# Kernel tuning notes

Hardware: AMD Instinct MI355X
Metric: run time of the kernel (lower is better)

## Reference

```python
import jax, jax.numpy as jnp
import numpy as np

N = 20000          # nodes
E_RAND = 320000    # random edges (avg degree 16)
E = E_RAND + N     # + self loops (no 0-in-degree nodes)
F_IN = 128
H1, D1 = 8, 32     # layer-1 heads / per-head dim
N_CLS = 40
NEG_SLOPE = 0.2


def setup_inputs() -> dict:
    key = jax.random.key(0)
    ks = jax.random.split(key, 9)
    x = jax.random.normal(ks[0], (N, F_IN), jnp.float32)
    src = jnp.concatenate([jax.random.randint(ks[1], (E_RAND,), 0, N),
                           jnp.arange(N)]).astype(jnp.int32)
    dst = jnp.concatenate([jax.random.randint(ks[2], (E_RAND,), 0, N),
                           jnp.arange(N)]).astype(jnp.int32)
    W1 = jax.random.normal(ks[3], (F_IN, H1 * D1), jnp.float32) / np.sqrt(F_IN)
    attn_l1 = jax.random.normal(ks[4], (H1, D1), jnp.float32) * 0.1
    attn_r1 = jax.random.normal(ks[5], (H1, D1), jnp.float32) * 0.1
    W2 = jax.random.normal(ks[6], (H1 * D1, N_CLS), jnp.float32) / np.sqrt(H1 * D1)
    attn_l2 = jax.random.normal(ks[7], (1, N_CLS), jnp.float32) * 0.1
    attn_r2 = jax.random.normal(ks[8], (1, N_CLS), jnp.float32) * 0.1
    return {"x": x, "W1": W1, "attn_l1": attn_l1, "attn_r1": attn_r1,
            "W2": W2, "attn_l2": attn_l2, "attn_r2": attn_r2,
            "src": src, "dst": dst}


def gat_layer(h, W, attn_l, attn_r, src, dst, n_nodes):
    """DGL GATConv (aggr='mean' path), eval mode (dropout = identity)."""
    H, D = attn_l.shape
    ft = (h @ W).reshape(-1, H, D)                 # [N, H, D]
    el = jnp.sum(ft * attn_l, axis=-1)             # [N, H]
    er = jnp.sum(ft * attn_r, axis=-1)             # [N, H]
    e = jax.nn.leaky_relu(el[src] + er[dst], NEG_SLOPE)   # [E, H]
    # ragged softmax over incoming edges of each dst node
    m = jax.ops.segment_max(e, dst, num_segments=n_nodes)
    m = jnp.where(jnp.isfinite(m), m, 0.0)         # guard empty segments
    ex = jnp.exp(e - m[dst])                       # [E, H]
    s = jax.ops.segment_sum(ex, dst, num_segments=n_nodes)
    alpha = ex / jnp.maximum(s[dst], 1e-16)        # [E, H]
    # weighted sum of src features
    out = jax.ops.segment_sum(ft[src] * alpha[:, :, None], dst,
                              num_segments=n_nodes)  # [N, H, D]
    return out


def reference(x, W1, attn_l1, attn_r1, W2, attn_l2, attn_r2, src, dst):
    h = gat_layer(x, W1, attn_l1, attn_r1, src, dst, N)   # [N, 8, 32]
    h = jax.nn.relu(h).reshape(N, H1 * D1)                # flatten(1)
    out = gat_layer(h, W2, attn_l2, attn_r2, src, dst, N) # [N, 1, 40]
    return out.mean(axis=1)                               # [N, 40]
```

## Files before the change

kernel.cpp:

```cpp
#include <hip/hip_runtime.h>
#include <hip/hip_fp16.h>

#define FIN 128
#define F1 256
#define H1N 8
#define D1N 32
#define NCLS 40
#define FT2P 64
#define NEG 0.2f

static __device__ __forceinline__ float leaky(float x){ return x >= 0.f ? x : NEG*x; }

__global__ void k_hist(const int* __restrict__ dst, int* __restrict__ deg, int E){
    int e = blockIdx.x*256 + threadIdx.x;
    if (e < E) atomicAdd(&deg[dst[e]], 1);
}

__global__ __launch_bounds__(1024) void k_scan(const int* __restrict__ deg,
                                               int* __restrict__ rowptr,
                                               int n, int E){
    __shared__ int s[1024];
    int t = threadIdx.x;
    int per = (n + 1023) / 1024;
    int base = t * per;
    int sum = 0;
    for (int i = 0; i < per; i++){
        int idx = base + i;
        if (idx < n) sum += deg[idx];
    }
    s[t] = sum;
    __syncthreads();
    for (int off = 1; off < 1024; off <<= 1){
        int v = (t >= off) ? s[t-off] : 0;
        __syncthreads();
        s[t] += v;
        __syncthreads();
    }
    int run = s[t] - sum;
    for (int i = 0; i < per; i++){
        int idx = base + i;
        if (idx < n){ rowptr[idx] = run; run += deg[idx]; }
    }
    if (t == 1023) rowptr[n] = E;
}

__global__ void k_scatter(const int* __restrict__ src, const int* __restrict__ dst,
                          const int* __restrict__ rowptr, int* __restrict__ deg,
                          int* __restrict__ adj, int E){
    int e = blockIdx.x*256 + threadIdx.x;
    if (e < E){
        int d = dst[e];
        int pos = atomicSub(&deg[d], 1) - 1;
        adj[rowptr[d] + pos] = src[e];
    }
}

__global__ __launch_bounds__(256) void k_gemm1(const float* __restrict__ X,
                                               const float* __restrict__ W,
                                               const float* __restrict__ al,
                                               const float* __restrict__ ar,
                                               __half* __restrict__ FT,
                                               float* __restrict__ el,
                                               float* __restrict__ er, int M){
    __shared__ float As[32][68];
    __shared__ float Bs[32][68];
    int t = threadIdx.x;
    int bx = blockIdx.x & 3;
    int by = blockIdx.x >> 2;
    int m0 = by*64, n0 = bx*64;
    int ty = t >> 4, tx = t & 15;
    float acc[4][4] = {};
    for (int k0 = 0; k0 < FIN; k0 += 32){
        #pragma unroll
        for (int p=0;p<2;p++){
            int f = t + p*256;
            int m = f >> 3;
            int kq = f & 7;
            int row = m0 + m;
            float4 v = make_float4(0.f,0.f,0.f,0.f);
            if (row < M) v = *(const float4*)&X[row*FIN + k0 + kq*4];
            As[kq*4+0][m] = v.x; As[kq*4+1][m] = v.y;
            As[kq*4+2][m] = v.z; As[kq*4+3][m] = v.w;
        }
        #pragma unroll
        for (int p=0;p<2;p++){
            int f = t + p*256;
            int kk = f >> 4;
            int nq = f & 15;
            float4 v = *(const float4*)&W[(size_t)(k0+kk)*F1 + n0 + nq*4];
            *(float4*)&Bs[kk][nq*4] = v;
        }
        __syncthreads();
        #pragma unroll
        for (int kk=0; kk<32; kk++){
            float4 a4 = *(const float4*)&As[kk][ty*4];
            float4 b4 = *(const float4*)&Bs[kk][tx*4];
            float av[4] = {a4.x,a4.y,a4.z,a4.w};
            float bv[4] = {b4.x,b4.y,b4.z,b4.w};
            #pragma unroll
            for (int r=0;r<4;r++)
                #pragma unroll
                for (int c=0;c<4;c++)
                    acc[r][c] = fmaf(av[r], bv[c], acc[r][c]);
        }
        __syncthreads();
    }
    int h = (bx<<1) + (tx>>3);
    int basew = h*D1N + (tx&7)*4;
    float4 wl = *(const float4*)&al[basew];
    float4 wr = *(const float4*)&ar[basew];
    float pl[4], pr[4];
    #pragma unroll
    for (int r=0;r<4;r++){
        pl[r] = acc[r][0]*wl.x + acc[r][1]*wl.y + acc[r][2]*wl.z + acc[r][3]*wl.w;
        pr[r] = acc[r][0]*wr.x + acc[r][1]*wr.y + acc[r][2]*wr.z + acc[r][3]*wr.w;
    }
    #pragma unroll
    for (int msk=1; msk<8; msk<<=1){
        #pragma unroll
        for (int r=0;r<4;r++){
            pl[r] += __shfl_xor(pl[r], msk);
            pr[r] += __shfl_xor(pr[r], msk);
        }
    }
    #pragma unroll
    for (int r=0;r<4;r++){
        int row = m0 + ty*4 + r;
        if (row < M){
            union { uint2 u; __half2 h2[2]; } P;
            P.h2[0] = __floats2half2_rn(acc[r][0], acc[r][1]);
            P.h2[1] = __floats2half2_rn(acc[r][2], acc[r][3]);
            *(uint2*)&FT[(size_t)row*F1 + n0 + tx*4] = P.u;
            if ((tx & 7) == 0){
                el[row*H1N + h] = pl[r];
                er[row*H1N + h] = pr[r];
            }
        }
    }
}

__global__ __launch_bounds__(256) void k_agg1(const __half* __restrict__ FT,
                      const float* __restrict__ el, const float* __restrict__ er,
                      const int* __restrict__ rowptr, const int* __restrict__ adj,
                      float* __restrict__ hout, int n){
    int node = (blockIdx.x*256 + threadIdx.x) >> 6;
    int l = threadIdx.x & 63;
    if (node >= n) return;
    int rs = rowptr[node];
    int deg = rowptr[node+1] - rs;

    int h = l & 7, je = l >> 3;
    float erh = er[node*H1N + h];
    float m = -1e30f, ssum = 0.f;
    for (int j0 = 0; j0 < deg; j0 += 8){
        int j = j0 + je;
        if (j < deg){
            int s = adj[rs + j];
            float e = leaky(el[s*H1N + h] + erh);
            if (e > m){ ssum = ssum*__expf(m - e) + 1.f; m = e; }
            else ssum += __expf(e - m);
        }
    }
    #pragma unroll
    for (int msk=8; msk<64; msk<<=1){
        float m2 = __shfl_xor(m, msk);
        float s2 = __shfl_xor(ssum, msk);
        float nm = fmaxf(m, m2);
        ssum = ssum*__expf(m - nm) + s2*__expf(m2 - nm);
        m = nm;
    }

    int h2 = l >> 3;
    float m2 = __shfl(m, h2);
    float s2 = __shfl(ssum, h2);
    float inv = 1.f / fmaxf(s2, 1e-16f);
    float erh2 = er[node*H1N + h2];
    float ax=0.f, ay=0.f, az=0.f, aw=0.f;
    int j = 0;
    for (; j + 8 <= deg; j += 8){
        int sv[8];
        #pragma unroll
        for (int i=0;i<8;i++) sv[i] = adj[rs+j+i];
        float av[8];
        #pragma unroll
        for (int i=0;i<8;i++)
            av[i] = __expf(leaky(el[sv[i]*H1N + h2] + erh2) - m2);
        #pragma unroll
        for (int i=0;i<8;i++){
            union { uint2 u; __half2 h2v[2]; } U;
            U.u = *(const uint2*)&FT[(size_t)sv[i]*F1 + l*4];
            float2 f01 = __half22float2(U.h2v[0]);
            float2 f23 = __half22float2(U.h2v[1]);
            ax = fmaf(av[i], f01.x, ax); ay = fmaf(av[i], f01.y, ay);
            az = fmaf(av[i], f23.x, az); aw = fmaf(av[i], f23.y, aw);
        }
    }
    for (; j < deg; j++){
        int s = adj[rs + j];
        float a = __expf(leaky(el[s*H1N + h2] + erh2) - m2);
        union { uint2 u; __half2 h2v[2]; } U;
        U.u = *(const uint2*)&FT[(size_t)s*F1 + l*4];
        float2 f01 = __half22float2(U.h2v[0]);
        float2 f23 = __half22float2(U.h2v[1]);
        ax = fmaf(a, f01.x, ax); ay = fmaf(a, f01.y, ay);
        az = fmaf(a, f23.x, az); aw = fmaf(a, f23.y, aw);
    }
    ax *= inv; ay *= inv; az *= inv; aw *= inv;
    *(float4*)&hout[(size_t)node*F1 + l*4] =
        make_float4(fmaxf(ax,0.f), fmaxf(ay,0.f), fmaxf(az,0.f), fmaxf(aw,0.f));
}

__global__ __launch_bounds__(256) void k_gemm2(const float* __restrict__ Hm,
                                               const float* __restrict__ W,
                                               const float* __restrict__ al2,
                                               const float* __restrict__ ar2,
                                               __half* __restrict__ FT2,
                                               float* __restrict__ el2,
                                               float* __restrict__ er2, int M){
    __shared__ float W2s[F1*NCLS];
    __shared__ float hs[128][33];
    int t = threadIdx.x;
    for (int i = t; i < F1*NCLS; i += 256) W2s[i] = W[i];
    int r0 = blockIdx.x*128;
    int rr = t & 63;
    int cg = t >> 6;
    int c0 = cg*10;
    float acc[2][10] = {};
    for (int k0 = 0; k0 < F1; k0 += 32){
        __syncthreads();
        #pragma unroll
        for (int p=0;p<4;p++){
            int f = t + p*256;
            int row = f >> 3;
            int kq = f & 7;
            int gr = r0 + row;
            float4 v = make_float4(0.f,0.f,0.f,0.f);
            if (gr < M) v = *(const float4*)&Hm[(size_t)gr*F1 + k0 + kq*4];
            hs[row][kq*4+0] = v.x; hs[row][kq*4+1] = v.y;
            hs[row][kq*4+2] = v.z; hs[row][kq*4+3] = v.w;
        }
        __syncthreads();
        #pragma unroll
        for (int k=0;k<32;k++){
            float a0 = hs[rr][k], a1 = hs[rr+64][k];
            const float* wp = &W2s[(k0+k)*NCLS + c0];
            #pragma unroll
            for (int c=0;c<10;c+=2){
                float2 w = *(const float2*)&wp[c];
                acc[0][c]   = fmaf(a0, w.x, acc[0][c]);
                acc[0][c+1] = fmaf(a0, w.y, acc[0][c+1]);
                acc[1][c]   = fmaf(a1, w.x, acc[1][c]);
                acc[1][c+1] = fmaf(a1, w.y, acc[1][c+1]);
            }
        }
    }
    float pl[2] = {0.f,0.f}, pr[2] = {0.f,0.f};
    #pragma unroll
    for (int c=0;c<10;c++){
        float a2l = al2[c0+c], a2r = ar2[c0+c];
        pl[0] = fmaf(acc[0][c], a2l, pl[0]); pr[0] = fmaf(acc[0][c], a2r, pr[0]);
        pl[1] = fmaf(acc[1][c], a2l, pl[1]); pr[1] = fmaf(acc[1][c], a2r, pr[1]);
    }
    #pragma unroll
    for (int i=0;i<2;i++){
        int gr = r0 + rr + i*64;
        if (gr < M){
            #pragma unroll
            for (int c=0;c<10;c+=2){
                __half2 hp = __floats2half2_rn(acc[i][c], acc[i][c+1]);
                *(__half2*)&FT2[(size_t)gr*FT2P + c0 + c] = hp;
            }
            atomicAdd(&el2[gr], pl[i]);
            atomicAdd(&er2[gr], pr[i]);
        }
    }
}

__global__ __launch_bounds__(256) void k_agg2(const __half* __restrict__ FT2,
                      const float* __restrict__ el, const float* __restrict__ er,
                      const int* __restrict__ rowptr, const int* __restrict__ adj,
                      float* __restrict__ out, int n){
    int node = (blockIdx.x*256 + threadIdx.x) >> 6;
    int l = threadIdx.x & 63;
    if (node >= n) return;
    int rs = rowptr[node];
    int deg = rowptr[node+1] - rs;
    float ern = er[node];
    float m = -1e30f, ssum = 0.f;
    for (int j = l; j < deg; j += 64){
        int s = adj[rs + j];
        float e = leaky(el[s] + ern);
        if (e > m){ ssum = ssum*__expf(m - e) + 1.f; m = e; }
        else ssum += __expf(e - m);
    }
    #pragma unroll
    for (int msk=1; msk<64; msk<<=1){
        float mm = __shfl_xor(m, msk);
        float s2 = __shfl_xor(ssum, msk);
        float nm = fmaxf(m, mm);
        ssum = ssum*__expf(m - nm) + s2*__expf(mm - nm);
        m = nm;
    }
    float inv = 1.f / fmaxf(ssum, 1e-16f);
    float acc = 0.f;
    int j = 0;
    for (; j + 8 <= deg; j += 8){
        int sv[8];
        #pragma unroll
        for (int i=0;i<8;i++) sv[i] = adj[rs+j+i];
        float av[8];
        #pragma unroll
        for (int i=0;i<8;i++)
            av[i] = __expf(leaky(el[sv[i]] + ern) - m);
        if (l < NCLS){
            #pragma unroll
            for (int i=0;i<8;i++){
                float f = __half2float(FT2[(size_t)sv[i]*FT2P + l]);
                acc = fmaf(av[i], f, acc);
            }
        }
    }
    for (; j < deg; j++){
        int s = adj[rs + j];
        float a = __expf(leaky(el[s] + ern) - m);
        if (l < NCLS) acc = fmaf(a, __half2float(FT2[(size_t)s*FT2P + l]), acc);
    }
    if (l < NCLS) out[(size_t)node*NCLS + l] = acc * inv;
}

extern "C" void kernel_launch(void* const* d_in, const int* in_sizes, int n_in,
                              void* d_out, int out_size, void* d_ws, size_t ws_size,
                              hipStream_t stream){
    const float* x   = (const float*)d_in[0];
    const float* W1  = (const float*)d_in[1];
    const float* al1 = (const float*)d_in[2];
    const float* ar1 = (const float*)d_in[3];
    const float* W2  = (const float*)d_in[4];
    const float* al2 = (const float*)d_in[5];
    const float* ar2 = (const float*)d_in[6];
    const int*   src = (const int*)d_in[7];
    const int*   dst = (const int*)d_in[8];
    int E = in_sizes[7];
    int n = in_sizes[0] / FIN;

    char* ws = (char*)d_ws;
    size_t off = 0;
    auto alloc = [&](size_t bytes)->void*{
        void* p = ws + off; off += (bytes + 255) & ~(size_t)255; return p;
    };
    __half* ft1h  = (__half*)alloc((size_t)n*F1*2);
    float*  hbuf  = (float*)alloc((size_t)n*F1*4);
    __half* ft2h  = (__half*)alloc((size_t)n*FT2P*2);
    float*  el1   = (float*)alloc((size_t)n*H1N*4);
    float*  er1   = (float*)alloc((size_t)n*H1N*4);
    int*    rowptr= (int*)alloc((size_t)(n+1)*4);
    int*    adj   = (int*)alloc((size_t)E*4);
    size_t  z0    = off;
    int*    deg   = (int*)alloc((size_t)n*4);
    float*  el2   = (float*)alloc((size_t)n*4);
    float*  er2   = (float*)alloc((size_t)n*4);
    size_t  z1    = off;

    int nb_e = (E + 255)/256;

    hipMemsetAsync(ws + z0, 0, z1 - z0, stream);
    k_hist   <<<nb_e, 256, 0, stream>>>(dst, deg, E);
    k_scan   <<<1, 1024, 0, stream>>>(deg, rowptr, n, E);
    k_scatter<<<nb_e, 256, 0, stream>>>(src, dst, rowptr, deg, adj, E);

    k_gemm1  <<<((n+63)/64)*4, 256, 0, stream>>>(x, W1, al1, ar1, ft1h, el1, er1, n);
    k_agg1   <<<(n+3)/4, 256, 0, stream>>>(ft1h, el1, er1, rowptr, adj, hbuf, n);

    k_gemm2  <<<(n+127)/128, 256, 0, stream>>>(hbuf, W2, al2, ar2, ft2h, el2, er2, n);
    k_agg2   <<<(n+3)/4, 256, 0, stream>>>(ft2h, el2, er2, rowptr, adj, (float*)d_out, n);
}
```

Before: 245.8 us.

## Fuse layer-2 GEMM into layer-1 aggregation and parallelize the degree scan

The layer-1 aggregation kernel now also multiplies each node's 256-wide ReLU output by W2, held in shared memory as fp16. It writes FT2 and el2/er2 directly, so the fp32 hidden buffer no longer round-trips through global memory and the separate GEMM2 kernel and its atomics are gone. The single-block 1024-thread scan is replaced with a two-kernel multi-block scan. The aggregation kernel now uses a persistent grid-stride loop over 2500 blocks. In exchange, each wave does a serial 256-long dot product per node, W2 is staged per block, and fp16 W2 adds some precision loss.

Result: faster. 212.1 us (-13.7%).

```diff
diff --git a/kernel.cpp b/kernel.cpp
--- a/kernel.cpp
+++ b/kernel.cpp
@@ -7,6 +7,7 @@
 #define D1N 32
 #define NCLS 40
 #define FT2P 64
+#define W2PITCH 260
 #define NEG 0.2f
 
 static __device__ __forceinline__ float leaky(float x){ return x >= 0.f ? x : NEG*x; }
@@ -16,32 +17,34 @@
     if (e < E) atomicAdd(&deg[dst[e]], 1);
 }
 
-__global__ __launch_bounds__(1024) void k_scan(const int* __restrict__ deg,
-                                               int* __restrict__ rowptr,
-                                               int n, int E){
-    __shared__ int s[1024];
+__global__ void k_scan1(const int* __restrict__ deg, int* __restrict__ rowptr,
+                        int* __restrict__ bsum, int n){
+    __shared__ int s[256];
     int t = threadIdx.x;
-    int per = (n + 1023) / 1024;
-    int base = t * per;
-    int sum = 0;
-    for (int i = 0; i < per; i++){
-        int idx = base + i;
-        if (idx < n) sum += deg[idx];
-    }
-    s[t] = sum;
+    int i = blockIdx.x*256 + t;
+    int v = (i < n) ? deg[i] : 0;
+    s[t] = v;
     __syncthreads();
-    for (int off = 1; off < 1024; off <<= 1){
-        int v = (t >= off) ? s[t-off] : 0;
+    for (int off=1; off<256; off<<=1){
+        int y = (t >= off) ? s[t-off] : 0;
         __syncthreads();
-        s[t] += v;
+        if (t >= off) s[t] += y;
         __syncthreads();
     }
-    int run = s[t] - sum;
-    for (int i = 0; i < per; i++){
-        int idx = base + i;
-        if (idx < n){ rowptr[idx] = run; run += deg[idx]; }
-    }
-    if (t == 1023) rowptr[n] = E;
+    if (i < n) rowptr[i] = s[t] - v;
+    if (t == 255) bsum[blockIdx.x] = s[255];
+}
+
+__global__ void k_scan2(int* __restrict__ rowptr, const int* __restrict__ bsum,
+                        int n, int E){
+    int b = blockIdx.x;
+    int l = threadIdx.x & 63;
+    int v = 0;
+    for (int j = l; j < b; j += 64) v += bsum[j];
+    for (int msk=1; msk<64; msk<<=1) v += __shfl_xor(v, msk);
+    int i = b*256 + threadIdx.x;
+    if (i < n) rowptr[i] += v;
+    else if (i == n) rowptr[n] = E;
 }
 
 __global__ void k_scatter(const int* __restrict__ src, const int* __restrict__ dst,
@@ -141,138 +144,113 @@
 
 __global__ __launch_bounds__(256) void k_agg1(const __half* __restrict__ FT,
                       const float* __restrict__ el, const float* __restrict__ er,
+                      const float* __restrict__ W2,
+                      const float* __restrict__ al2, const float* __restrict__ ar2,
                       const int* __restrict__ rowptr, const int* __restrict__ adj,
-                      float* __restrict__ hout, int n){
-    int node = (blockIdx.x*256 + threadIdx.x) >> 6;
-    int l = threadIdx.x & 63;
-    if (node >= n) return;
-    int rs = rowptr[node];
-    int deg = rowptr[node+1] - rs;
-
+                      __half* __restrict__ FT2, float* __restrict__ el2,
+                      float* __restrict__ er2, int n, int nwTot){
+    __shared__ __half W2h[40*W2PITCH];
+    __shared__ float  hst[4][260];
+    int t = threadIdx.x;
+    for (int e = t; e < 256*40; e += 256){
+        int k = e / 40, c = e - k*40;
+        W2h[c*W2PITCH + k] = __float2half_rn(W2[e]);
+    }
+    __syncthreads();
+
+    int w = t >> 6, l = t & 63;
     int h = l & 7, je = l >> 3;
-    float erh = er[node*H1N + h];
-    float m = -1e30f, ssum = 0.f;
-    for (int j0 = 0; j0 < deg; j0 += 8){
-        int j = j0 + je;
-        if (j < deg){
+    int h2 = l >> 3;
+    int c = (l < 40) ? l : (l - 40);
+    float keep = (l < NCLS) ? 1.f : 0.f;
+    float a2l = al2[c], a2r = ar2[c];
+    const __half* wrow = &W2h[c*W2PITCH];
+    float* hp = &hst[w][0];
+
+    for (int node = blockIdx.x*4 + w; node < n; node += nwTot){
+        int rs = rowptr[node];
+        int deg = rowptr[node+1] - rs;
+
+        float erh = er[node*H1N + h];
+        float m = -1e30f, ssum = 0.f;
+        for (int j0 = 0; j0 < deg; j0 += 8){
+            int j = j0 + je;
+            if (j < deg){
+                int s = adj[rs + j];
+                float e = leaky(el[s*H1N + h] + erh);
+                if (e > m){ ssum = ssum*__expf(m - e) + 1.f; m = e; }
+                else ssum += __expf(e - m);
+            }
+        }
+        #pragma unroll
+        for (int msk=8; msk<64; msk<<=1){
+            float m2 = __shfl_xor(m, msk);
+            float s2 = __shfl_xor(ssum, msk);
+            float nm = fmaxf(m, m2);
+            ssum = ssum*__expf(m - nm) + s2*__expf(m2 - nm);
+            m = nm;
+        }
+
+        float m2 = __shfl(m, h2);
+        float s2 = __shfl(ssum, h2);
+        float inv = 1.f / fmaxf(s2, 1e-16f);
+        float erh2 = er[node*H1N + h2];
+        float ax=0.f, ay=0.f, az=0.f, aw=0.f;
+        int j = 0;
+        for (; j + 8 <= deg; j += 8){
+            int sv[8];
+            #pragma unroll
+            for (int i=0;i<8;i++) sv[i] = adj[rs+j+i];
+            float av[8];
+            #pragma unroll
+            for (int i=0;i<8;i++)
+                av[i] = __expf(leaky(el[sv[i]*H1N + h2] + erh2) - m2);
+            #pragma unroll
+            for (int i=0;i<8;i++){
+                union { uint2 u; __half2 h2v[2]; } U;
+                U.u = *(const uint2*)&FT[(size_t)sv[i]*F1 + l*4];
+                float2 f01 = __half22float2(U.h2v[0]);
+                float2 f23 = __half22float2(U.h2v[1]);
+                ax = fmaf(av[i], f01.x, ax); ay = fmaf(av[i], f01.y, ay);
+                az = fmaf(av[i], f23.x, az); aw = fmaf(av[i], f23.y, aw);
+            }
+        }
+        for (; j < deg; j++){
             int s = adj[rs + j];
-            float e = leaky(el[s*H1N + h] + erh);
-            if (e > m){ ssum = ssum*__expf(m - e) + 1.f; m = e; }
-            else ssum += __expf(e - m);
-        }
-    }
-    #pragma unroll
-    for (int msk=8; msk<64; msk<<=1){
-        float m2 = __shfl_xor(m, msk);
-        float s2 = __shfl_xor(ssum, msk);
-        float nm = fmaxf(m, m2);
-        ssum = ssum*__expf(m - nm) + s2*__expf(m2 - nm);
-        m = nm;
-    }
-
-    int h2 = l >> 3;
-    float m2 = __shfl(m, h2);
-    float s2 = __shfl(ssum, h2);
-    float inv = 1.f / fmaxf(s2, 1e-16f);
-    float erh2 = er[node*H1N + h2];
-    float ax=0.f, ay=0.f, az=0.f, aw=0.f;
-    int j = 0;
-    for (; j + 8 <= deg; j += 8){
-        int sv[8];
-        #pragma unroll
-        for (int i=0;i<8;i++) sv[i] = adj[rs+j+i];
-        float av[8];
-        #pragma unroll
-        for (int i=0;i<8;i++)
-            av[i] = __expf(leaky(el[sv[i]*H1N + h2] + erh2) - m2);
-        #pragma unroll
-        for (int i=0;i<8;i++){
+            float a = __expf(leaky(el[s*H1N + h2] + erh2) - m2);
             union { uint2 u; __half2 h2v[2]; } U;
-            U.u = *(const uint2*)&FT[(size_t)sv[i]*F1 + l*4];
+            U.u = *(const uint2*)&FT[(size_t)s*F1 + l*4];
             float2 f01 = __half22float2(U.h2v[0]);
             float2 f23 = __half22float2(U.h2v[1]);
-            ax = fmaf(av[i], f01.x, ax); ay = fmaf(av[i], f01.y, ay);
-            az = fmaf(av[i], f23.x, az); aw = fmaf(av[i], f23.y, aw);
-        }
-    }
-    for (; j < deg; j++){
-        int s = adj[rs + j];
-        float a = __expf(leaky(el[s*H1N + h2] + erh2) - m2);
-        union { uint2 u; __half2 h2v[2]; } U;
-        U.u = *(const uint2*)&FT[(size_t)s*F1 + l*4];
-        float2 f01 = __half22float2(U.h2v[0]);
-        float2 f23 = __half22float2(U.h2v[1]);
-        ax = fmaf(a, f01.x, ax); ay = fmaf(a, f01.y, ay);
-        az = fmaf(a, f23.x, az); aw = fmaf(a, f23.y, aw);
-    }
-    ax *= inv; ay *= inv; az *= inv; aw *= inv;
-    *(float4*)&hout[(size_t)node*F1 + l*4] =
-        make_float4(fmaxf(ax,0.f), fmaxf(ay,0.f), fmaxf(az,0.f), fmaxf(aw,0.f));
-}
-
-__global__ __launch_bounds__(256) void k_gemm2(const float* __restrict__ Hm,
-                                               const float* __restrict__ W,
-                                               const float* __restrict__ al2,
-                                               const float* __restrict__ ar2,
-                                               __half* __restrict__ FT2,
-                                               float* __restrict__ el2,
-                                               float* __restrict__ er2, int M){
-    __shared__ float W2s[F1*NCLS];
-    __shared__ float hs[128][33];
-    int t = threadIdx.x;
-    for (int i = t; i < F1*NCLS; i += 256) W2s[i] = W[i];
-    int r0 = blockIdx.x*128;
-    int rr = t & 63;
-    int cg = t >> 6;
-    int c0 = cg*10;
-    float acc[2][10] = {};
-    for (int k0 = 0; k0 < F1; k0 += 32){
-        __syncthreads();
-        #pragma unroll
-        for (int p=0;p<4;p++){
-            int f = t + p*256;
-            int row = f >> 3;
-            int kq = f & 7;
-            int gr = r0 + row;
-            float4 v = make_float4(0.f,0.f,0.f,0.f);
-            if (gr < M) v = *(const float4*)&Hm[(size_t)gr*F1 + k0 + kq*4];
-            hs[row][kq*4+0] = v.x; hs[row][kq*4+1] = v.y;
-            hs[row][kq*4+2] = v.z; hs[row][kq*4+3] = v.w;
-        }
-        __syncthreads();
-        #pragma unroll
-        for (int k=0;k<32;k++){
-            float a0 = hs[rr][k], a1 = hs[rr+64][k];
-            const float* wp = &W2s[(k0+k)*NCLS + c0];
-            #pragma unroll
-            for (int c=0;c<10;c+=2){
-                float2 w = *(const float2*)&wp[c];
-                acc[0][c]   = fmaf(a0, w.x, acc[0][c]);
-                acc[0][c+1] = fmaf(a0, w.y, acc[0][c+1]);
-                acc[1][c]   = fmaf(a1, w.x, acc[1][c]);
-                acc[1][c+1] = fmaf(a1, w.y, acc[1][c+1]);
-            }
-        }
-    }
-    float pl[2] = {0.f,0.f}, pr[2] = {0.f,0.f};
-    #pragma unroll
-    for (int c=0;c<10;c++){
-        float a2l = al2[c0+c], a2r = ar2[c0+c];
-        pl[0] = fmaf(acc[0][c], a2l, pl[0]); pr[0] = fmaf(acc[0][c], a2r, pr[0]);
-        pl[1] = fmaf(acc[1][c], a2l, pl[1]); pr[1] = fmaf(acc[1][c], a2r, pr[1]);
-    }
-    #pragma unroll
-    for (int i=0;i<2;i++){
-        int gr = r0 + rr + i*64;
-        if (gr < M){
-            #pragma unroll
-            for (int c=0;c<10;c+=2){
-                __half2 hp = __floats2half2_rn(acc[i][c], acc[i][c+1]);
-                *(__half2*)&FT2[(size_t)gr*FT2P + c0 + c] = hp;
-            }
-            atomicAdd(&el2[gr], pl[i]);
-            atomicAdd(&er2[gr], pr[i]);
-        }
+            ax = fmaf(a, f01.x, ax); ay = fmaf(a, f01.y, ay);
+            az = fmaf(a, f23.x, az); aw = fmaf(a, f23.y, aw);
+        }
+        ax = fmaxf(ax*inv, 0.f); ay = fmaxf(ay*inv, 0.f);
+        az = fmaxf(az*inv, 0.f); aw = fmaxf(aw*inv, 0.f);
+
+        *(float4*)&hp[l*4] = make_float4(ax, ay, az, aw);
+        __builtin_amdgcn_wave_barrier();
+        asm volatile("s_waitcnt lgkmcnt(0)" ::: "memory");
+        float out = 0.f;
+        #pragma unroll 8
+        for (int k0 = 0; k0 < 64; k0++){
+            float4 hv = *(const float4*)&hp[k0*4];
+            __half2 wa = *(const __half2*)&wrow[k0*4];
+            __half2 wb = *(const __half2*)&wrow[k0*4+2];
+            float2 fa = __half22float2(wa), fb = __half22float2(wb);
+            out = fmaf(hv.x, fa.x, out); out = fmaf(hv.y, fa.y, out);
+            out = fmaf(hv.z, fb.x, out); out = fmaf(hv.w, fb.y, out);
+        }
+        __builtin_amdgcn_wave_barrier();
+        float pl = keep * out * a2l;
+        float pr = keep * out * a2r;
+        #pragma unroll
+        for (int msk=1; msk<64; msk<<=1){
+            pl += __shfl_xor(pl, msk);
+            pr += __shfl_xor(pr, msk);
+        }
+        if (l == 0){ el2[node] = pl; er2[node] = pr; }
+        if (l < NCLS) FT2[(size_t)node*FT2P + l] = __float2half_rn(out);
     }
 }
 
@@ -349,28 +327,31 @@
         void* p = ws + off; off += (bytes + 255) & ~(size_t)255; return p;
     };
     __half* ft1h  = (__half*)alloc((size_t)n*F1*2);
-    float*  hbuf  = (float*)alloc((size_t)n*F1*4);
     __half* ft2h  = (__half*)alloc((size_t)n*FT2P*2);
     float*  el1   = (float*)alloc((size_t)n*H1N*4);
     float*  er1   = (float*)alloc((size_t)n*H1N*4);
+    float*  el2   = (float*)alloc((size_t)n*4);
+    float*  er2   = (float*)alloc((size_t)n*4);
     int*    rowptr= (int*)alloc((size_t)(n+1)*4);
     int*    adj   = (int*)alloc((size_t)E*4);
-    size_t  z0    = off;
+    int*    bsum  = (int*)alloc((size_t)((n+255)/256)*4);
     int*    deg   = (int*)alloc((size_t)n*4);
-    float*  el2   = (float*)alloc((size_t)n*4);
-    float*  er2   = (float*)alloc((size_t)n*4);
-    size_t  z1    = off;
 
     int nb_e = (E + 255)/256;
-
-    hipMemsetAsync(ws + z0, 0, z1 - z0, stream);
+    int nb_n = (n + 255)/256;
+
+    hipMemsetAsync(deg, 0, (size_t)n*4, stream);
     k_hist   <<<nb_e, 256, 0, stream>>>(dst, deg, E);
-    k_scan   <<<1, 1024, 0, stream>>>(deg, rowptr, n, E);
+    k_scan1  <<<nb_n, 256, 0, stream>>>(deg, rowptr, bsum, n);
+    k_scan2  <<<(n+1+255)/256, 256, 0, stream>>>(rowptr, bsum, n, E);
     k_scatter<<<nb_e, 256, 0, stream>>>(src, dst, rowptr, deg, adj, E);
 
     k_gemm1  <<<((n+63)/64)*4, 256, 0, stream>>>(x, W1, al1, ar1, ft1h, el1, er1, n);
-    k_agg1   <<<(n+3)/4, 256, 0, stream>>>(ft1h, el1, er1, rowptr, adj, hbuf, n);
-
-    k_gemm2  <<<(n+127)/128, 256, 0, stream>>>(hbuf, W2, al2, ar2, ft2h, el2, er2, n);
-    k_agg2   <<<(n+3)/4, 256, 0, stream>>>(ft2h, el2, er2, rowptr, adj, (float*)d_out, n);
-}
+
+    int aggBlocks = 2500;
+    k_agg1   <<<aggBlocks, 256, 0, stream>>>(ft1h, el1, er1, W2, al2, ar2,
+                                             rowptr, adj, ft2h, el2, er2,
+                                             n, aggBlocks*4);
+    k_agg2   <<<(n+3)/4, 256, 0, stream>>>(ft2h, el2, er2, rowptr, adj,
+                                           (float*)d_out, n);
+}
```
